# Kernel tuning notes

Measured on AMD Instinct MI355X. Metric: run time of the kernel, lower is better.

## Reference

```python
import jax, jax.numpy as jnp
import numpy as np

NUM_GROUPS = 32
EPS = 1e-6
HEAD = 8


def group_norm(x, gamma, beta):
    # x: (b, c, h, w); normalize per group of channels over (c/g, h, w)
    b, c, h, w = x.shape
    g = NUM_GROUPS
    xg = x.reshape(b, g, c // g, h, w)
    mean = xg.mean(axis=(2, 3, 4), keepdims=True)
    var = xg.var(axis=(2, 3, 4), keepdims=True)
    xn = ((xg - mean) * jax.lax.rsqrt(var + EPS)).reshape(b, c, h, w)
    return xn * gamma[None, :, None, None] + beta[None, :, None, None]


def setup_inputs() -> dict:
    key = jax.random.key(0)
    ks = jax.random.split(key, 6)
    b, c, h, w = 8, 512, 64, 64
    sd = 1.0 / np.sqrt(c)
    return {
        "x": jax.random.normal(ks[0], (b, c, h, w), jnp.float32),
        "gamma": jnp.ones((c,), jnp.float32),
        "beta": jnp.zeros((c,), jnp.float32),
        "Wq": jax.random.normal(ks[1], (c, c), jnp.float32) * sd,
        "Wk": jax.random.normal(ks[2], (c, c), jnp.float32) * sd,
        "Wv": jax.random.normal(ks[3], (c, c), jnp.float32) * sd,
        "Wp": jax.random.normal(ks[4], (c, c), jnp.float32) * sd,
        "bp": jnp.zeros((c,), jnp.float32),
    }


def reference(x, gamma, beta, Wq, Wk, Wv, Wp, bp):
    b, c, h, w = x.shape
    hd = c // HEAD
    scale = jnp.sqrt(jnp.float32(hd))  # NOTE: original MULTIPLIES by sqrt(d)
    xn = group_norm(x, gamma, beta)            # (b, c, h, w)
    x_ = xn.reshape(b, c, h * w).transpose(0, 2, 1)  # (b, n, c), n = h*w
    # torch Linear: y = x @ W.T
    Q = (x_ @ Wq.T).reshape(b, h * w, HEAD, hd)
    K = (x_ @ Wk.T).reshape(b, h * w, HEAD, hd)
    V = (x_ @ Wv.T).reshape(b, h * w, HEAD, hd)
    # einsum 'bhid,bhjd->bhij' with axes (b, n, head, hd): per-position head gram
    dots = jnp.einsum('bnid,bnjd->bnij', Q, K) * scale  # (b, n, head, head)
    att = jax.nn.softmax(dots, axis=1)  # softmax over the SPATIAL axis (dim=1)
    out = jnp.einsum('bnij,bnjd->bnid', att, V).reshape(b, h * w, c)
    out = out @ Wp.T + bp  # dropout is identity at inference
    return out.transpose(0, 2, 1).reshape(b, c, h, w) + xn  # residual adds normed x
```

## Files before the change

kernel.cpp:

```cpp
#include <hip/hip_runtime.h>
#include <stdint.h>

typedef unsigned short ushort_t;
typedef _Float16 half8 __attribute__((ext_vector_type(8)));
typedef float f32x4 __attribute__((ext_vector_type(4)));

#define GLOBAL_AS __attribute__((address_space(1)))
#define LDS_AS    __attribute__((address_space(3)))

__device__ __forceinline__ float bf2f(ushort_t u) {
    union { unsigned i; float f; } v; v.i = ((unsigned)u) << 16; return v.f;
}
__device__ __forceinline__ ushort_t f2h(float f) {
    union { _Float16 h; ushort_t u; } v; v.h = (_Float16)f; return v.u;
}
__device__ __forceinline__ float h2f(ushort_t u) {
    union { _Float16 h; ushort_t u; } v; v.u = u; return (float)v.h;
}

__device__ __forceinline__ void async16(const void* g, void* l) {
    __builtin_amdgcn_global_load_lds((const GLOBAL_AS uint32_t*)g,
                                     (LDS_AS uint32_t*)l, 16, 0, 0);
}

__device__ __forceinline__ int is_bf16_in(const uint32_t* g32) {
    return *g32 == 0x3F803F80u;
}

__global__ __launch_bounds__(256) void prep(const void* Wq, const void* Wk,
                                            const void* Wv, const void* Wp,
                                            const void* g, const void* be, const void* bp,
                                            ushort_t* Wh, float* gcan, float* bcan,
                                            float* bpcan, const uint32_t* g32) {
    const int id = blockIdx.x;
    const int isbf = is_bf16_in(g32);
    if (id < 512) {
        const int wsel = id >> 7, wblk = id & 127;
        const void* src = (wsel == 0) ? Wq : (wsel == 1) ? Wk : (wsel == 2) ? Wv : Wp;
        ushort_t* dst = Wh + (size_t)wsel * 262144;
        const int e0 = wblk * 2048 + threadIdx.x * 8;
        ushort_t o[8];
        if (isbf) {
            uint4 u = *(const uint4*)((const ushort_t*)src + e0);
            const ushort_t* e = (const ushort_t*)&u;
#pragma unroll
            for (int j = 0; j < 8; ++j) o[j] = f2h(bf2f(e[j]));
        } else {
            float4 a = *(const float4*)((const float*)src + e0);
            float4 b = *(const float4*)((const float*)src + e0 + 4);
            o[0] = f2h(a.x); o[1] = f2h(a.y); o[2] = f2h(a.z); o[3] = f2h(a.w);
            o[4] = f2h(b.x); o[5] = f2h(b.y); o[6] = f2h(b.z); o[7] = f2h(b.w);
        }
        *(uint4*)(dst + e0) = *(const uint4*)o;
    } else {
        int t = threadIdx.x + (id - 512) * 256;
        if (isbf) {
            gcan[t]  = bf2f(((const ushort_t*)g)[t]);
            bcan[t]  = bf2f(((const ushort_t*)be)[t]);
            bpcan[t] = bf2f(((const ushort_t*)bp)[t]);
        } else {
            gcan[t]  = ((const float*)g)[t];
            bcan[t]  = ((const float*)be)[t];
            bpcan[t] = ((const float*)bp)[t];
        }
    }
}

__global__ __launch_bounds__(256) void gn_part(const void* xv, float* __restrict__ psums,
                                               const uint32_t* g32) {
    const int bx = blockIdx.x, t = threadIdx.x;
    const size_t base = (size_t)(bx >> 3) * 65536 + (size_t)(bx & 7) * 8192;
    float s = 0.f, sq = 0.f;
    if (is_bf16_in(g32)) {
        const ushort_t* p = (const ushort_t*)xv + base;
        for (int i = 0; i < 4; ++i) {
            uint4 u = ((const uint4*)p)[t + 256 * i];
            const ushort_t* e = (const ushort_t*)&u;
#pragma unroll
            for (int j = 0; j < 8; ++j) { float f = bf2f(e[j]); s += f; sq += f * f; }
        }
    } else {
        const float* p = (const float*)xv + base;
        for (int i = 0; i < 8; ++i) {
            float4 v = ((const float4*)p)[t + 256 * i];
            s += v.x + v.y + v.z + v.w;
            sq += v.x * v.x + v.y * v.y + v.z * v.z + v.w * v.w;
        }
    }
    __shared__ float ls[256], lq[256];
    ls[t] = s; lq[t] = sq;
    __syncthreads();
    for (int off = 128; off > 0; off >>= 1) {
        if (t < off) { ls[t] += ls[t + off]; lq[t] += lq[t + off]; }
        __syncthreads();
    }
    if (t == 0) { psums[bx * 2] = ls[0]; psums[bx * 2 + 1] = lq[0]; }
}

__global__ __launch_bounds__(256) void gn_apply_t(const void* xv,
                                                  const float* __restrict__ gcan,
                                                  const float* __restrict__ bcan,
                                                  const float* __restrict__ psums,
                                                  ushort_t* __restrict__ xnt,
                                                  ushort_t* __restrict__ xnc,
                                                  const uint32_t* g32) {
    const int nt = blockIdx.x;
    const int ct = blockIdx.y;
    const int b  = blockIdx.z;
    const int t  = threadIdx.x;
    const int c0 = ct * 64, n0 = nt * 64;
    __shared__ __align__(16) ushort_t tile[64 * 80];
    __shared__ float scS[64], shS[64];
    if (t < 64) {
        int c = c0 + t;
        int g = c >> 4;
        float s = 0.f, q = 0.f;
#pragma unroll
        for (int k = 0; k < 8; ++k) {
            s += psums[((b * 32 + g) * 8 + k) * 2];
            q += psums[((b * 32 + g) * 8 + k) * 2 + 1];
        }
        float mean = s * (1.f / 65536.f);
        float var  = q * (1.f / 65536.f) - mean * mean;
        float rstd = rsqrtf(fmaxf(var, 0.f) + 1e-6f);
        float sc = rstd * gcan[c];
        scS[t] = sc;
        shS[t] = bcan[c] - mean * sc;
    }
    __syncthreads();
    if (is_bf16_in(g32)) {
        const ushort_t* x = (const ushort_t*)xv;
#pragma unroll
        for (int p = 0; p < 2; ++p) {
            int u = p * 256 + t;
            int cc = u >> 3, nc = u & 7;
            int c = c0 + cc;
            size_t gidx = ((size_t)(b * 512 + c)) * 4096 + n0 + nc * 8;
            uint4 raw = *(const uint4*)(x + gidx);
            float sc = scS[cc], sh = shS[cc];
            const ushort_t* e = (const ushort_t*)&raw;
            ushort_t hv[8];
#pragma unroll
            for (int j = 0; j < 8; ++j) {
                hv[j] = f2h(bf2f(e[j]) * sc + sh);
                tile[(nc * 8 + j) * 80 + cc] = hv[j];
            }
            *(uint4*)(xnc + gidx) = *(const uint4*)hv;
        }
    } else {
        const float* x = (const float*)xv;
#pragma unroll
        for (int p = 0; p < 4; ++p) {
            int u = p * 256 + t;
            int cc = u >> 4, nc = u & 15;
            int c = c0 + cc;
            size_t gidx = ((size_t)(b * 512 + c)) * 4096 + n0 + nc * 4;
            float4 raw = *(const float4*)(x + gidx);
            float sc = scS[cc], sh = shS[cc];
            ushort_t hv[4];
            hv[0] = f2h(raw.x * sc + sh);
            hv[1] = f2h(raw.y * sc + sh);
            hv[2] = f2h(raw.z * sc + sh);
            hv[3] = f2h(raw.w * sc + sh);
#pragma unroll
            for (int j = 0; j < 4; ++j) tile[(nc * 4 + j) * 80 + cc] = hv[j];
            *(uint2*)(xnc + gidx) = *(const uint2*)hv;
        }
    }
    __syncthreads();
#pragma unroll
    for (int p = 0; p < 2; ++p) {
        int u = p * 256 + t;
        int nn = u >> 3, cchunk = u & 7;
        uint4 o = *(const uint4*)(tile + nn * 80 + cchunk * 8);
        *(uint4*)(xnt + ((size_t)(b * 4096 + n0 + nn)) * 512 + c0 + cchunk * 8) = o;
    }
}

__device__ __forceinline__ void mfma_tile(const ushort_t* Ab, const ushort_t* Bb,
                                          int wm, int wn, int lr, int qe,
                                          f32x4 acc[4][4]) {
    half8 af[4], bf[4];
#pragma unroll
    for (int mi = 0; mi < 4; ++mi)
        af[mi] = *(const half8*)(Ab + (wm + mi * 16 + lr) * 32 + qe * 8);
#pragma unroll
    for (int ni = 0; ni < 4; ++ni)
        bf[ni] = *(const half8*)(Bb + (wn + ni * 16 + lr) * 32 + qe * 8);
#pragma unroll
    for (int mi = 0; mi < 4; ++mi)
#pragma unroll
        for (int ni = 0; ni < 4; ++ni)
            acc[mi][ni] = __builtin_amdgcn_mfma_f32_16x16x32_f16(af[mi], bf[ni],
                                                                 acc[mi][ni], 0, 0, 0);
}

__device__ __forceinline__ void gemm128_core(const ushort_t* __restrict__ A,
                                             const ushort_t* __restrict__ B,
                                             int m0, int n0, int K, f32x4 acc[4][4]) {
    __shared__ __align__(16) ushort_t As[2][128 * 32];
    __shared__ __align__(16) ushort_t Bs[2][128 * 32];
    const int t = threadIdx.x;
    const int l = t & 63;
    const int w = t >> 6;
    const int wm = (w >> 1) * 64, wn = (w & 1) * 64;
    const int lr = l & 15, q = l >> 4;
    const int qe = q ^ ((lr >> 1) & 3);
    const int r0 = t >> 2;
    const int kc = (t & 3) ^ ((r0 >> 1) & 3);
    const ushort_t* gA0 = A + (size_t)(m0 + r0) * K + kc * 8;
    const ushort_t* gB0 = B + (size_t)(n0 + r0) * K + kc * 8;
    const ushort_t* gA1 = gA0 + (size_t)64 * K;
    const ushort_t* gB1 = gB0 + (size_t)64 * K;

    f32x4 zero = {0.f, 0.f, 0.f, 0.f};
#pragma unroll
    for (int mi = 0; mi < 4; ++mi)
#pragma unroll
        for (int ni = 0; ni < 4; ++ni) acc[mi][ni] = zero;

    {
        char* sA = (char*)&As[0][0] + w * 1024;
        char* sB = (char*)&Bs[0][0] + w * 1024;
        async16(gA0, sA); async16(gA1, sA + 4096);
        async16(gB0, sB); async16(gB1, sB + 4096);
    }
    asm volatile("s_waitcnt vmcnt(0)" ::: "memory");
    __builtin_amdgcn_s_barrier();

    int cur = 0;
    for (int kt = 32; kt < K; kt += 32) {
        char* sA = (char*)&As[cur ^ 1][0] + w * 1024;
        char* sB = (char*)&Bs[cur ^ 1][0] + w * 1024;
        async16(gA0 + kt, sA); async16(gA1 + kt, sA + 4096);
        async16(gB0 + kt, sB); async16(gB1 + kt, sB + 4096);
        mfma_tile(&As[cur][0], &Bs[cur][0], wm, wn, lr, qe, acc);
        asm volatile("s_waitcnt vmcnt(0)" ::: "memory");
        __builtin_amdgcn_s_barrier();
        cur ^= 1;
    }
    mfma_tile(&As[cur][0], &Bs[cur][0], wm, wn, lr, qe, acc);
}

__global__ __launch_bounds__(256) void gemm_qkv(const ushort_t* __restrict__ xnt,
                                                const ushort_t* __restrict__ Wh,
                                                ushort_t* __restrict__ Qo,
                                                ushort_t* __restrict__ Ko,
                                                ushort_t* __restrict__ Vo) {
    const int id = blockIdx.x;
    const int xcd = id & 7, s = id >> 3;
    const int mloc = s / 12, r = s % 12;
    const int m0 = (xcd * 32 + mloc) * 128;
    const int n0 = (r & 3) * 128;
    const int z  = r >> 2;
    const ushort_t* B = Wh + (size_t)z * 262144;
    ushort_t* C = (z == 0) ? Qo : (z == 1) ? Ko : Vo;
    f32x4 acc[4][4];
    gemm128_core(xnt, B, m0, n0, 512, acc);
    const int t = threadIdx.x, l = t & 63, w = t >> 6;
    const int wm = (w >> 1) * 64, wn = (w & 1) * 64;
    const int col = l & 15, q = l >> 4;
#pragma unroll
    for (int mi = 0; mi < 4; ++mi)
#pragma unroll
        for (int ni = 0; ni < 4; ++ni)
#pragma unroll
            for (int rr = 0; rr < 4; ++rr) {
                int row = wm + mi * 16 + q * 4 + rr;
                int cc  = wn + ni * 16 + col;
                C[(size_t)(m0 + row) * 512 + n0 + cc] = f2h(acc[mi][ni][rr]);
            }
}

__global__ __launch_bounds__(256) void dots_smax(const ushort_t* __restrict__ Q,
                                                 const ushort_t* __restrict__ K,
                                                 float* __restrict__ dots,
                                                 float* __restrict__ pmax,
                                                 float* __restrict__ psum) {
    const int chunk = blockIdx.x;
    const int t = threadIdx.x, l = t & 63, w = t >> 6;
    const int m = l & 15, q = l >> 4, col = m;
    __shared__ float sd[128][64];
    __shared__ float lm[4][64], lsum[4][64];
#pragma unroll
    for (int i = 0; i < 16; ++i) {
        int gpl = (i * 4 + w) * 2;
        int gp0 = chunk * 128 + gpl;
        const size_t base = (size_t)(gp0 + (m >> 3)) * 512 + (m & 7) * 64 + q * 8;
        half8 a0 = *(const half8*)(Q + base);
        half8 a1 = *(const half8*)(Q + base + 32);
        half8 b0 = *(const half8*)(K + base);
        half8 b1 = *(const half8*)(K + base + 32);
        f32x4 acc = {0.f, 0.f, 0.f, 0.f};
        acc = __builtin_amdgcn_mfma_f32_16x16x32_f16(a0, b0, acc, 0, 0, 0);
        acc = __builtin_amdgcn_mfma_f32_16x16x32_f16(a1, b1, acc, 0, 0, 0);
#pragma unroll
        for (int r = 0; r < 4; ++r) {
            int row = q * 4 + r;
            if (row < 8 && col < 8) {
                float v = acc[r] * 8.0f;
                int ij = row * 8 + col;
                sd[gpl][ij] = v;
                dots[(size_t)(gp0)*64 + ij] = v;
            }
            if (row >= 8 && col >= 8) {
                float v = acc[r] * 8.0f;
                int ij = (row - 8) * 8 + (col - 8);
                sd[gpl + 1][ij] = v;
                dots[(size_t)(gp0 + 1) * 64 + ij] = v;
            }
        }
    }
    __syncthreads();
    const int ij = l;
    float mx = -1e30f;
    float v[32];
#pragma unroll
    for (int r = 0; r < 32; ++r) { v[r] = sd[w * 32 + r][ij]; mx = fmaxf(mx, v[r]); }
    lm[w][ij] = mx;
    __syncthreads();
    float cm = fmaxf(fmaxf(lm[0][ij], lm[1][ij]), fmaxf(lm[2][ij], lm[3][ij]));
    float sum = 0.f;
#pragma unroll
    for (int r = 0; r < 32; ++r) sum += __expf(v[r] - cm);
    lsum[w][ij] = sum;
    __syncthreads();
    if (w == 0) {
        pmax[chunk * 64 + ij] = cm;
        psum[chunk * 64 + ij] = lsum[0][ij] + lsum[1][ij] + lsum[2][ij] + lsum[3][ij];
    }
}

__global__ __launch_bounds__(256) void attn_apply(const float* __restrict__ dots,
                                                  const float* __restrict__ pmax,
                                                  const float* __restrict__ psum,
                                                  const ushort_t* __restrict__ V,
                                                  ushort_t* __restrict__ P) {
    const int t = threadIdx.x, l = t & 63, w = t >> 6;
    const int gp_base = blockIdx.x * 16;
    const int b = gp_base >> 12;
    __shared__ float pm4[4][64], ps4[4][64];
    __shared__ float Mv[64], Siv[64];
    {
        const int cg = w * 8;
        float m = -1e30f;
        float pmv[8], psv[8];
#pragma unroll
        for (int c = 0; c < 8; ++c) {
            pmv[c] = pmax[(b * 32 + cg + c) * 64 + l];
            psv[c] = psum[(b * 32 + cg + c) * 64 + l];
            m = fmaxf(m, pmv[c]);
        }
        float s = 0.f;
#pragma unroll
        for (int c = 0; c < 8; ++c) s += psv[c] * __expf(pmv[c] - m);
        pm4[w][l] = m; ps4[w][l] = s;
    }
    __syncthreads();
    if (w == 0) {
        float M = fmaxf(fmaxf(pm4[0][l], pm4[1][l]), fmaxf(pm4[2][l], pm4[3][l]));
        float S = ps4[0][l] * __expf(pm4[0][l] - M) + ps4[1][l] * __expf(pm4[1][l] - M)
                + ps4[2][l] * __expf(pm4[2][l] - M) + ps4[3][l] * __expf(pm4[3][l] - M);
        Mv[l] = M;
        Siv[l] = 1.f / S;
    }
    __syncthreads();
    const float mv = Mv[l], siv = Siv[l];
    __shared__ float att[4][64];
    __shared__ __align__(16) ushort_t vb[4][512];
    const int i = l >> 3, dc = l & 7;
    for (int p = 0; p < 4; ++p) {
        int gp = gp_base + w * 4 + p;
        float d = dots[(size_t)gp * 64 + l];
        att[w][l] = __expf(d - mv) * siv;
        *(uint4*)(&vb[w][l * 8]) = *(const uint4*)(V + (size_t)gp * 512 + l * 8);
        float o[8] = {0, 0, 0, 0, 0, 0, 0, 0};
#pragma unroll
        for (int j = 0; j < 8; ++j) {
            float a = att[w][i * 8 + j];
            uint4 vv = *(const uint4*)(&vb[w][j * 64 + dc * 8]);
            const ushort_t* ve = (const ushort_t*)&vv;
#pragma unroll
            for (int k2 = 0; k2 < 8; ++k2) o[k2] += a * h2f(ve[k2]);
        }
        ushort_t ou[8];
#pragma unroll
        for (int k2 = 0; k2 < 8; ++k2) ou[k2] = f2h(o[k2]);
        *(uint4*)(P + (size_t)gp * 512 + l * 8) = *(const uint4*)ou;
    }
}

__global__ __launch_bounds__(256) void gemm_out(const ushort_t* __restrict__ Wph,
                                                const ushort_t* __restrict__ P,
                                                const ushort_t* __restrict__ xnc,
                                                const float* __restrict__ bpcan,
                                                float* __restrict__ out) {
    const int id = blockIdx.x;
    const int xcd = id & 7, s = id >> 3;
    const int pair = xcd * 32 + (s >> 2);
    const int o0 = (s & 3) * 128;
    const int b  = pair >> 5;
    const int n0 = (pair & 31) * 128;
    f32x4 acc[4][4];
    gemm128_core(Wph, P + (size_t)b * 4096 * 512, o0, n0, 512, acc);
    const int t = threadIdx.x, l = t & 63, w = t >> 6;
    const int wm = (w >> 1) * 64, wn = (w & 1) * 64;
    const int col = l & 15, q = l >> 4;
#pragma unroll
    for (int mi = 0; mi < 4; ++mi) {
#pragma unroll
        for (int r = 0; r < 4; ++r) {
            int o = o0 + wm + mi * 16 + q * 4 + r;
            float bias = bpcan[o];
#pragma unroll
            for (int ni = 0; ni < 4; ++ni) {
                int n = n0 + wn + ni * 16 + col;
                size_t idx = ((size_t)(b * 512 + o)) * 4096 + n;
                out[idx] = acc[mi][ni][r] + bias + h2f(xnc[idx]);
            }
        }
    }
}

extern "C" void kernel_launch(void* const* d_in, const int* in_sizes, int n_in,
                              void* d_out, int out_size, void* d_ws, size_t ws_size,
                              hipStream_t stream) {
    const void* x     = d_in[0];
    const void* gamma = d_in[1];
    const void* beta  = d_in[2];
    const void* Wq    = d_in[3];
    const void* Wk    = d_in[4];
    const void* Wv    = d_in[5];
    const void* Wp    = d_in[6];
    const void* bp    = d_in[7];
    const uint32_t* g32 = (const uint32_t*)gamma;
    float* out = (float*)d_out;

    char* ws = (char*)d_ws;
    const size_t SZ = 33554432;
    ushort_t* xnt = (ushort_t*)(ws);
    ushort_t* Qh  = (ushort_t*)(ws + 1 * SZ);
    ushort_t* Kh  = (ushort_t*)(ws + 2 * SZ);
    ushort_t* Vh  = (ushort_t*)(ws + 3 * SZ);
    float* dots   = (float*)(ws + 4 * SZ);
    ushort_t* Wh  = (ushort_t*)(ws + 4 * SZ + 8388608);
    ushort_t* xnc = (ushort_t*)(ws + 4 * SZ + 8388608 + 2097152);
    char* tail    = ws + 4 * SZ + 8388608 + 2097152 + SZ;
    float* gcan   = (float*)(tail);
    float* bcan   = gcan + 512;
    float* bpcan  = bcan + 512;
    float* psums  = bpcan + 512;
    float* pmax   = psums + 4096;
    float* psumS  = pmax + 16384;
    ushort_t* Pb  = xnt;

    prep      <<<514, 256, 0, stream>>>(Wq, Wk, Wv, Wp, gamma, beta, bp,
                                        Wh, gcan, bcan, bpcan, g32);
    gn_part   <<<2048, 256, 0, stream>>>(x, psums, g32);
    gn_apply_t<<<dim3(64, 8, 8), 256, 0, stream>>>(x, gcan, bcan, psums, xnt, xnc, g32);
    gemm_qkv  <<<3072, 256, 0, stream>>>(xnt, Wh, Qh, Kh, Vh);
    dots_smax <<<256, 256, 0, stream>>>(Qh, Kh, dots, pmax, psumS);
    attn_apply<<<2048, 256, 0, stream>>>(dots, pmax, psumS, Vh, Pb);
    gemm_out  <<<1024, 256, 0, stream>>>(Wh + 3 * 262144, Pb, xnc, bpcan, out);
}
```

Baseline: 309.2 us.

## Triple-buffer GEMM LDS tiles with partial vmcnt waits to deepen prefetch

Replaces the double-buffered K loop in the shared 128x128 GEMM core with a three-stage ring buffer. Two tiles stay in flight while the current one is computed, using partial vmcnt waits instead of draining all loads. Fragments are read from LDS first, then a barrier lets the freed slot be refilled before the MFMAs are issued. This hides more global-load latency, at the cost of 50% more LDS per block, which may lower occupancy, plus an extra barrier per iteration.

```diff
diff --git a/kernel.cpp b/kernel.cpp
--- a/kernel.cpp
+++ b/kernel.cpp
@@ -177,29 +177,11 @@
     }
 }
 
-__device__ __forceinline__ void mfma_tile(const ushort_t* Ab, const ushort_t* Bb,
-                                          int wm, int wn, int lr, int qe,
-                                          f32x4 acc[4][4]) {
-    half8 af[4], bf[4];
-#pragma unroll
-    for (int mi = 0; mi < 4; ++mi)
-        af[mi] = *(const half8*)(Ab + (wm + mi * 16 + lr) * 32 + qe * 8);
-#pragma unroll
-    for (int ni = 0; ni < 4; ++ni)
-        bf[ni] = *(const half8*)(Bb + (wn + ni * 16 + lr) * 32 + qe * 8);
-#pragma unroll
-    for (int mi = 0; mi < 4; ++mi)
-#pragma unroll
-        for (int ni = 0; ni < 4; ++ni)
-            acc[mi][ni] = __builtin_amdgcn_mfma_f32_16x16x32_f16(af[mi], bf[ni],
-                                                                 acc[mi][ni], 0, 0, 0);
-}
-
 __device__ __forceinline__ void gemm128_core(const ushort_t* __restrict__ A,
                                              const ushort_t* __restrict__ B,
                                              int m0, int n0, int K, f32x4 acc[4][4]) {
-    __shared__ __align__(16) ushort_t As[2][128 * 32];
-    __shared__ __align__(16) ushort_t Bs[2][128 * 32];
+    __shared__ __align__(16) ushort_t As[3][128 * 32];
+    __shared__ __align__(16) ushort_t Bs[3][128 * 32];
     const int t = threadIdx.x;
     const int l = t & 63;
     const int w = t >> 6;
@@ -219,27 +201,52 @@
 #pragma unroll
         for (int ni = 0; ni < 4; ++ni) acc[mi][ni] = zero;
 
-    {
-        char* sA = (char*)&As[0][0] + w * 1024;
-        char* sB = (char*)&Bs[0][0] + w * 1024;
-        async16(gA0, sA); async16(gA1, sA + 4096);
-        async16(gB0, sB); async16(gB1, sB + 4096);
-    }
-    asm volatile("s_waitcnt vmcnt(0)" ::: "memory");
+    const int NT = K >> 5;
+
+#pragma unroll
+    for (int pt = 0; pt < 3; ++pt) {
+        char* sA = (char*)&As[pt][0] + w * 1024;
+        char* sB = (char*)&Bs[pt][0] + w * 1024;
+        async16(gA0 + pt * 32, sA); async16(gA1 + pt * 32, sA + 4096);
+        async16(gB0 + pt * 32, sB); async16(gB1 + pt * 32, sB + 4096);
+    }
+    asm volatile("s_waitcnt vmcnt(8)" ::: "memory");
     __builtin_amdgcn_s_barrier();
 
-    int cur = 0;
-    for (int kt = 32; kt < K; kt += 32) {
-        char* sA = (char*)&As[cur ^ 1][0] + w * 1024;
-        char* sB = (char*)&Bs[cur ^ 1][0] + w * 1024;
-        async16(gA0 + kt, sA); async16(gA1 + kt, sA + 4096);
-        async16(gB0 + kt, sB); async16(gB1 + kt, sB + 4096);
-        mfma_tile(&As[cur][0], &Bs[cur][0], wm, wn, lr, qe, acc);
-        asm volatile("s_waitcnt vmcnt(0)" ::: "memory");
+    for (int tt = 0; tt < NT; ++tt) {
+        const int cur = tt % 3;
+        const ushort_t* Ab = &As[cur][0];
+        const ushort_t* Bb = &Bs[cur][0];
+        half8 af[4], bf[4];
+#pragma unroll
+        for (int mi = 0; mi < 4; ++mi)
+            af[mi] = *(const half8*)(Ab + (wm + mi * 16 + lr) * 32 + qe * 8);
+#pragma unroll
+        for (int ni = 0; ni < 4; ++ni)
+            bf[ni] = *(const half8*)(Bb + (wn + ni * 16 + lr) * 32 + qe * 8);
+        asm volatile("s_waitcnt lgkmcnt(0)" ::: "memory");
+        __builtin_amdgcn_sched_barrier(0);
         __builtin_amdgcn_s_barrier();
-        cur ^= 1;
-    }
-    mfma_tile(&As[cur][0], &Bs[cur][0], wm, wn, lr, qe, acc);
+        if (tt + 3 < NT) {
+            char* sA = (char*)&As[cur][0] + w * 1024;
+            char* sB = (char*)&Bs[cur][0] + w * 1024;
+            const int kt = (tt + 3) * 32;
+            async16(gA0 + kt, sA); async16(gA1 + kt, sA + 4096);
+            async16(gB0 + kt, sB); async16(gB1 + kt, sB + 4096);
+        }
+#pragma unroll
+        for (int mi = 0; mi < 4; ++mi)
+#pragma unroll
+            for (int ni = 0; ni < 4; ++ni)
+                acc[mi][ni] = __builtin_amdgcn_mfma_f32_16x16x32_f16(af[mi], bf[ni],
+                                                                     acc[mi][ni], 0, 0, 0);
+        if (tt + 1 < NT) {
+            if (tt + 3 < NT)      asm volatile("s_waitcnt vmcnt(8)" ::: "memory");
+            else if (tt + 2 < NT) asm volatile("s_waitcnt vmcnt(4)" ::: "memory");
+            else                  asm volatile("s_waitcnt vmcnt(0)" ::: "memory");
+            __builtin_amdgcn_s_barrier();
+        }
+    }
 }
 
 __global__ __launch_bounds__(256) void gemm_qkv(const ushort_t* __restrict__ xnt,
```

New measurement: 280.7 us. 1.1x faster.
